# Performance work log

Hardware: AMD Instinct MI355X
Metric: run time of the kernel (lower is better)

Reference implementation:

```python
import jax, jax.numpy as jnp
import numpy as np

H = 4          # heads (hardcoded in original forward via shp=(4, ...))
B, G, D = 2, 2048, 128
KD = VD = 32   # key_dim = val_dim = embed_dim // n_heads
E = 128        # embed_dim


def setup_inputs() -> dict:
    key = jax.random.key(0)
    ks = jax.random.split(key, 10)
    s = lambda d: 1.0 / np.sqrt(d)
    return {
        "h": jax.random.normal(ks[0], (B, G, D), jnp.float32),
        "out_source_attn": jax.random.normal(ks[1], (H, B, G, G), jnp.float32),
        "Wq": jax.random.uniform(ks[2], (H, D, KD), jnp.float32, -s(KD), s(KD)),
        "Wk": jax.random.uniform(ks[3], (H, D, KD), jnp.float32, -s(KD), s(KD)),
        "Wv": jax.random.uniform(ks[4], (H, D, VD), jnp.float32, -s(VD), s(VD)),
        "Wout": jax.random.uniform(ks[5], (H, KD, E), jnp.float32, -s(E), s(E)),
        "w1": jax.random.uniform(ks[6], (8, 8), jnp.float32, -s(8), s(8)),
        "b1": jax.random.uniform(ks[7], (8,), jnp.float32, -s(8), s(8)),
        "w2": jax.random.uniform(ks[8], (4, 8), jnp.float32, -s(8), s(8)),
        "b2": jax.random.uniform(ks[9], (4,), jnp.float32, -s(4), s(4)),
    }


def reference(h, out_source_attn, Wq, Wk, Wv, Wout, w1, b1, w2, b2):
    # Per-head projections: (H, B, G, kd/vd)
    Q = jnp.einsum('bgd,hdk->hbgk', h, Wq)
    K = jnp.einsum('bgd,hdk->hbgk', h, Wk)
    V = jnp.einsum('bgd,hdv->hbgv', h, Wv)
    # QK^T scores concat with external attention source: (2H=8, B, G, G)
    scores = jnp.einsum('hbqk,hbpk->hbqp', Q, K)
    compat = jnp.concatenate([scores, out_source_attn], axis=0)
    # Per-score small MLP (Linear(8,8)->ReLU->Linear(8,4)) over channel dim
    x = compat.transpose(1, 2, 3, 0)                 # (B, G, G, 8)
    x = jax.nn.relu(x @ w1.T + b1) @ w2.T + b2       # (B, G, G, 4)
    attn = jax.nn.softmax(x.transpose(3, 0, 1, 2), axis=-1)  # (H, B, G, G)
    heads = jnp.einsum('hbqp,hbpv->hbqv', attn, V)   # (H, B, G, VD)
    out = jnp.einsum('hbqv,hve->bqe', heads, Wout)   # (B, G, E)
    return (out, out_source_attn)
```

## Files before the change

### kernel.cpp

```cpp
#include <hip/hip_runtime.h>

typedef __attribute__((ext_vector_type(8))) short bf16x8;
typedef __attribute__((ext_vector_type(4))) short bf16x4;
typedef __attribute__((ext_vector_type(4))) float f32x4;

#define OUT0 524288
#define SRC_CH_STRIDE 8388608
#define PART_HEAD 544
#define PART_SLICE 2176
#define NSLICE 8

__device__ __forceinline__ unsigned short f2bf(float x){
    unsigned u = __builtin_bit_cast(unsigned, x);
    u += 0x7FFFu + ((u >> 16) & 1u);
    return (unsigned short)(u >> 16);
}

__device__ __forceinline__ f32x4 mfma16x16x16_bf16(bf16x4 a, bf16x4 b, f32x4 c){
#if __has_builtin(__builtin_amdgcn_mfma_f32_16x16x16bf16_1k)
    return __builtin_amdgcn_mfma_f32_16x16x16bf16_1k(a, b, c, 0, 0, 0);
#else
    f32x4 d;
    asm volatile("v_mfma_f32_16x16x16_bf16 %0, %1, %2, %3"
                 : "=v"(d) : "v"(a), "v"(b), "v"(c));
    return d;
#endif
}

__global__ __launch_bounds__(256) void qkv_kernel(
    const float* __restrict__ hsrc,
    const float* __restrict__ Wq, const float* __restrict__ Wk, const float* __restrict__ Wv,
    unsigned short* __restrict__ Qb, unsigned short* __restrict__ Kb, unsigned short* __restrict__ Vt)
{
    __shared__ float hs[32*128];
    __shared__ float ws[128*32];
    const int t = threadIdx.x;
    const int g0 = blockIdx.x * 32;
    const int mat = blockIdx.y;
    const int mt = mat >> 2, head = mat & 3;
    {
        const float4* s = (const float4*)(hsrc + g0*128);
        float4* d = (float4*)hs;
        #pragma unroll
        for (int i=0;i<4;i++) d[t + i*256] = s[t + i*256];
        const float* W = (mt==0?Wq:(mt==1?Wk:Wv)) + head*4096;
        const float4* s2 = (const float4*)W;
        float4* d2 = (float4*)ws;
        #pragma unroll
        for (int i=0;i<4;i++) d2[t + i*256] = s2[t + i*256];
    }
    __syncthreads();
    const int r = t >> 3;
    const int k0 = (t & 7) * 4;
    float a0=0.f,a1=0.f,a2=0.f,a3=0.f;
    const float* hr = hs + r*128;
    #pragma unroll 8
    for (int d=0; d<128; d++){
        float hv = hr[d];
        float4 w4 = *(const float4*)(ws + d*32 + k0);
        a0 = fmaf(hv, w4.x, a0); a1 = fmaf(hv, w4.y, a1);
        a2 = fmaf(hv, w4.z, a2); a3 = fmaf(hv, w4.w, a3);
    }
    const int row_g = g0 + r;
    if (mt == 2){
        const int b = row_g >> 11, g = row_g & 2047;
        unsigned short* dst = Vt + ((b*128 + head*32 + k0) * 2048) + g;
        dst[0] = f2bf(a0); dst[2048] = f2bf(a1); dst[4096] = f2bf(a2); dst[6144] = f2bf(a3);
    } else {
        unsigned short* dst = (mt==0?Qb:Kb) + row_g*128 + head*32 + k0;
        dst[0]=f2bf(a0); dst[1]=f2bf(a1); dst[2]=f2bf(a2); dst[3]=f2bf(a3);
    }
}

__global__ __launch_bounds__(256, 2) void attn_kernel(
    const float* __restrict__ src,
    const unsigned short* __restrict__ Qb,
    const unsigned short* __restrict__ Kb,
    const unsigned short* __restrict__ Vt,
    const float* __restrict__ w1g, const float* __restrict__ b1g,
    const float* __restrict__ w2g, const float* __restrict__ b2g,
    float* __restrict__ part,
    float* __restrict__ out)
{
    __shared__ __align__(16) float wt[112];

    const int t = threadIdx.x;
    const int lane = t & 63;
    const int wv = t >> 6;
    const int quad = lane >> 4;
    const int lrow = lane & 15;
    const int qt = blockIdx.x * 4 + wv;
    const int q0 = qt * 16;
    const int b = blockIdx.y;
    const int s = blockIdx.z;
    const int pbase = s * (2048 / NSLICE);

    if (t < 64) wt[t] = w1g[t];
    else if (t < 72) wt[t] = b1g[t-64];
    else if (t < 104){ const int j = (t-72) >> 2, cc = (t-72) & 3; wt[t] = w2g[cc*8 + j]; }
    else if (t < 108) wt[t] = b2g[t-104];

    bf16x8 qf[4];
    {
        const unsigned short* Qrow = Qb + (b*2048 + q0 + lrow)*128 + quad*8;
        #pragma unroll
        for (int h=0; h<4; h++) qf[h] = *(const bf16x8*)(Qrow + h*32);
    }

    const int rowbase = (b*2048 + q0 + lrow)*2048;
    const long vbase  = (long)(b*128)*2048;

    f32x4 o[4][2];
    float mreg[4], lreg[4];
    #pragma unroll
    for (int h=0; h<4; h++){
        o[h][0] = (f32x4){0.f,0.f,0.f,0.f};
        o[h][1] = (f32x4){0.f,0.f,0.f,0.f};
        mreg[h] = -1e30f; lreg[h] = 0.f;
    }
    const f32x4 zero4 = {0.f,0.f,0.f,0.f};

    __syncthreads();

    for (int it = 0; it < (2048/NSLICE)/16; ++it){
        const int p0 = pbase + it*16;

        float xr[4][4];
        {
            float4 r4[4];
            #pragma unroll
            for (int ch=0; ch<4; ch++)
                r4[ch] = *(const float4*)(src + ch*SRC_CH_STRIDE + rowbase + p0 + quad*4);
            #pragma unroll
            for (int ch=0; ch<4; ch++)
                *(float4*)(out + OUT0 + ch*SRC_CH_STRIDE + rowbase + p0 + quad*4) = r4[ch];
            #pragma unroll
            for (int ch=0; ch<4; ch++){
                xr[ch][0]=r4[ch].x; xr[ch][1]=r4[ch].y; xr[ch][2]=r4[ch].z; xr[ch][3]=r4[ch].w;
            }
        }

        bf16x4 vf[4][2];
        #pragma unroll
        for (int h=0; h<4; h++){
            #pragma unroll
            for (int half=0; half<2; half++)
                vf[h][half] = *(const bf16x4*)(Vt + vbase + (long)(h*32 + half*16 + lrow)*2048 + p0 + quad*4);
        }

        f32x4 sc[4];
        {
            const unsigned short* Krow = Kb + (b*2048 + p0 + lrow)*128 + quad*8;
            #pragma unroll
            for (int h=0; h<4; h++){
                const bf16x8 kf = *(const bf16x8*)(Krow + h*32);
                sc[h] = __builtin_amdgcn_mfma_f32_16x16x32_bf16(kf, qf[h], zero4, 0, 0, 0);
            }
        }

        float z[4][4];
        #pragma unroll
        for (int cc=0; cc<4; cc++){
            const float bb = wt[104+cc];
            #pragma unroll
            for (int r=0; r<4; r++) z[cc][r] = bb;
        }
        #pragma unroll
        for (int j=0; j<8; j++){
            const float4 wa  = *(const float4*)(wt + j*8);
            const float4 wb  = *(const float4*)(wt + j*8 + 4);
            const float  bj  = wt[64+j];
            const float4 w2r = *(const float4*)(wt + 72 + j*4);
            #pragma unroll
            for (int r=0; r<4; r++){
                float v = bj;
                v = fmaf(wa.x, sc[0][r], v);
                v = fmaf(wa.y, sc[1][r], v);
                v = fmaf(wa.z, sc[2][r], v);
                v = fmaf(wa.w, sc[3][r], v);
                v = fmaf(wb.x, xr[0][r], v);
                v = fmaf(wb.y, xr[1][r], v);
                v = fmaf(wb.z, xr[2][r], v);
                v = fmaf(wb.w, xr[3][r], v);
                v = fmaxf(v, 0.f);
                z[0][r] = fmaf(w2r.x, v, z[0][r]);
                z[1][r] = fmaf(w2r.y, v, z[1][r]);
                z[2][r] = fmaf(w2r.z, v, z[2][r]);
                z[3][r] = fmaf(w2r.w, v, z[3][r]);
            }
        }

        #pragma unroll
        for (int h=0; h<4; h++){
            float mloc = fmaxf(fmaxf(z[h][0], z[h][1]), fmaxf(z[h][2], z[h][3]));
            mloc = fmaxf(mloc, __shfl_xor(mloc, 16));
            mloc = fmaxf(mloc, __shfl_xor(mloc, 32));
            const float mn = fmaxf(mreg[h], mloc);
            const float e0 = __expf(z[h][0] - mn);
            const float e1 = __expf(z[h][1] - mn);
            const float e2 = __expf(z[h][2] - mn);
            const float e3 = __expf(z[h][3] - mn);
            float ss = (e0 + e1) + (e2 + e3);
            ss += __shfl_xor(ss, 16);
            ss += __shfl_xor(ss, 32);
            const float alpha = __expf(mreg[h] - mn);
            mreg[h] = mn;
            lreg[h] = fmaf(lreg[h], alpha, ss);
            o[h][0] *= alpha;
            o[h][1] *= alpha;
            bf16x4 pf;
            pf[0] = (short)f2bf(e0); pf[1] = (short)f2bf(e1);
            pf[2] = (short)f2bf(e2); pf[3] = (short)f2bf(e3);
            o[h][0] = mfma16x16x16_bf16(vf[h][0], pf, o[h][0]);
            o[h][1] = mfma16x16x16_bf16(vf[h][1], pf, o[h][1]);
        }
    }

    #pragma unroll
    for (int h=0; h<4; h++){
        float* P = part + (((b*128 + qt)*NSLICE + s)*4 + h) * PART_HEAD;
        if (quad == 0){
            P[lrow]      = mreg[h];
            P[16 + lrow] = lreg[h];
        }
        *(f32x4*)(P + 32 + lrow*32 +      quad*4) = o[h][0];
        *(f32x4*)(P + 32 + lrow*32 + 16 + quad*4) = o[h][1];
    }
}

__global__ __launch_bounds__(256) void combine_kernel(
    const float* __restrict__ part,
    const float* __restrict__ Wout,
    float* __restrict__ out)
{
    __shared__ __align__(16) float O_lds[64*33];
    const int t = threadIdx.x;
    const int qt = blockIdx.x, b = blockIdx.y;

    if (t < 64){
        const int c = t >> 4, q = t & 15;
        const float* P0 = part + (((b*128 + qt)*NSLICE + 0)*4 + c) * PART_HEAD;
        float m[NSLICE];
        #pragma unroll
        for (int j=0;j<NSLICE;j++) m[j] = P0[j*PART_SLICE + q];
        float M = m[0];
        #pragma unroll
        for (int j=1;j<NSLICE;j++) M = fmaxf(M, m[j]);
        float w[NSLICE];
        float L = 0.f;
        #pragma unroll
        for (int j=0;j<NSLICE;j++){
            w[j] = __expf(m[j] - M);
            L = fmaf(P0[j*PART_SLICE + 16 + q], w[j], L);
        }
        float invL = 1.f / L;
        const float* O0 = P0 + 32 + q*32;
        float* dst = O_lds + t*33;
        #pragma unroll
        for (int v4 = 0; v4 < 8; v4++){
            float ax=0.f, ay=0.f, az=0.f, aw=0.f;
            #pragma unroll
            for (int j=0;j<NSLICE;j++){
                float4 a = *(const float4*)(O0 + j*PART_SLICE + v4*4);
                ax = fmaf(a.x, w[j], ax);
                ay = fmaf(a.y, w[j], ay);
                az = fmaf(a.z, w[j], az);
                aw = fmaf(a.w, w[j], aw);
            }
            dst[v4*4+0] = ax * invL;
            dst[v4*4+1] = ay * invL;
            dst[v4*4+2] = az * invL;
            dst[v4*4+3] = aw * invL;
        }
    }
    __syncthreads();

    {
        const int mq = t >> 4;
        const int e0 = (t & 15) * 8;
        float acc[8];
        #pragma unroll
        for (int i=0;i<8;i++) acc[i]=0.f;
        #pragma unroll
        for (int cc=0; cc<4; cc++){
            const float* OhRow = O_lds + (cc*16 + mq)*33;
            const float* Wrow = Wout + cc*32*128 + e0;
            #pragma unroll 4
            for (int v=0; v<32; v++){
                float ov = OhRow[v];
                float4 wA = *(const float4*)(Wrow + v*128);
                float4 wB = *(const float4*)(Wrow + v*128 + 4);
                acc[0]=fmaf(ov,wA.x,acc[0]); acc[1]=fmaf(ov,wA.y,acc[1]);
                acc[2]=fmaf(ov,wA.z,acc[2]); acc[3]=fmaf(ov,wA.w,acc[3]);
                acc[4]=fmaf(ov,wB.x,acc[4]); acc[5]=fmaf(ov,wB.y,acc[5]);
                acc[6]=fmaf(ov,wB.z,acc[6]); acc[7]=fmaf(ov,wB.w,acc[7]);
            }
        }
        float* op = out + (b*2048 + qt*16 + mq)*128 + e0;
        float4 oA; oA.x=acc[0]; oA.y=acc[1]; oA.z=acc[2]; oA.w=acc[3];
        float4 oB; oB.x=acc[4]; oB.y=acc[5]; oB.z=acc[6]; oB.w=acc[7];
        *(float4*)op = oA;
        *(float4*)(op+4) = oB;
    }
}

extern "C" void kernel_launch(void* const* d_in, const int* in_sizes, int n_in,
                              void* d_out, int out_size, void* d_ws, size_t ws_size,
                              hipStream_t stream) {
    const float* h    = (const float*)d_in[0];
    const float* src  = (const float*)d_in[1];
    const float* Wq   = (const float*)d_in[2];
    const float* Wk   = (const float*)d_in[3];
    const float* Wv   = (const float*)d_in[4];
    const float* Wout = (const float*)d_in[5];
    const float* w1   = (const float*)d_in[6];
    const float* b1   = (const float*)d_in[7];
    const float* w2   = (const float*)d_in[8];
    const float* b2   = (const float*)d_in[9];
    float* out = (float*)d_out;

    unsigned short* Qb = (unsigned short*)d_ws;
    unsigned short* Kb = Qb + 524288;
    unsigned short* Vt = Kb + 524288;
    float* part = (float*)((char*)d_ws + 3*1048576);

    qkv_kernel<<<dim3(128,12), 256, 0, stream>>>(h, Wq, Wk, Wv, Qb, Kb, Vt);
    attn_kernel<<<dim3(32,2,NSLICE), 256, 0, stream>>>(src, Qb, Kb, Vt, w1, b1, w2, b2, part, out);
    combine_kernel<<<dim3(128,2), 256, 0, stream>>>(part, Wout, out);
}
```

Measured before the change: 387.9 us.

## Double-buffer source attention loads across 32-column pairs of subtiles

Restructures the main loop to prefetch the next 32 columns of out_source_attn into registers, using two ping-pong buffers, while the current pair of 16-column subtiles is computed. The copy-out store and the loads are issued ahead of the MLP and softmax work to hide global memory latency. This adds register pressure from holding 32 extra floats per buffer, which could reduce occupancy.

```diff
diff --git a/kernel.cpp b/kernel.cpp
--- a/kernel.cpp
+++ b/kernel.cpp
@@ -120,34 +120,21 @@
     }
     const f32x4 zero4 = {0.f,0.f,0.f,0.f};
 
-    __syncthreads();
-
-    for (int it = 0; it < (2048/NSLICE)/16; ++it){
-        const int p0 = pbase + it*16;
-
-        float xr[4][4];
-        {
-            float4 r4[4];
+    auto pairload = [&](float4 (&buf)[2][4], int pb){
+        #pragma unroll
+        for (int s2=0; s2<2; s2++)
             #pragma unroll
             for (int ch=0; ch<4; ch++)
-                r4[ch] = *(const float4*)(src + ch*SRC_CH_STRIDE + rowbase + p0 + quad*4);
+                buf[s2][ch] = *(const float4*)(src + ch*SRC_CH_STRIDE + rowbase + pb + s2*16 + quad*4);
+    };
+    auto pairstore = [&](float4 (&buf)[2][4], int pb){
+        #pragma unroll
+        for (int s2=0; s2<2; s2++)
             #pragma unroll
             for (int ch=0; ch<4; ch++)
-                *(float4*)(out + OUT0 + ch*SRC_CH_STRIDE + rowbase + p0 + quad*4) = r4[ch];
-            #pragma unroll
-            for (int ch=0; ch<4; ch++){
-                xr[ch][0]=r4[ch].x; xr[ch][1]=r4[ch].y; xr[ch][2]=r4[ch].z; xr[ch][3]=r4[ch].w;
-            }
-        }
-
-        bf16x4 vf[4][2];
-        #pragma unroll
-        for (int h=0; h<4; h++){
-            #pragma unroll
-            for (int half=0; half<2; half++)
-                vf[h][half] = *(const bf16x4*)(Vt + vbase + (long)(h*32 + half*16 + lrow)*2048 + p0 + quad*4);
-        }
-
+                *(float4*)(out + OUT0 + ch*SRC_CH_STRIDE + rowbase + pb + s2*16 + quad*4) = buf[s2][ch];
+    };
+    auto subtile = [&](int p0, const float4* x4){
         f32x4 sc[4];
         {
             const unsigned short* Krow = Kb + (b*2048 + p0 + lrow)*128 + quad*8;
@@ -157,7 +144,18 @@
                 sc[h] = __builtin_amdgcn_mfma_f32_16x16x32_bf16(kf, qf[h], zero4, 0, 0, 0);
             }
         }
-
+        bf16x4 vf[4][2];
+        #pragma unroll
+        for (int h=0; h<4; h++)
+            #pragma unroll
+            for (int hf=0; hf<2; hf++)
+                vf[h][hf] = *(const bf16x4*)(Vt + vbase + (long)(h*32 + hf*16 + lrow)*2048 + p0 + quad*4);
+
+        float xr[4][4];
+        #pragma unroll
+        for (int ch=0; ch<4; ch++){
+            xr[ch][0]=x4[ch].x; xr[ch][1]=x4[ch].y; xr[ch][2]=x4[ch].z; xr[ch][3]=x4[ch].w;
+        }
         float z[4][4];
         #pragma unroll
         for (int cc=0; cc<4; cc++){
@@ -189,7 +187,6 @@
                 z[3][r] = fmaf(w2r.w, v, z[3][r]);
             }
         }
-
         #pragma unroll
         for (int h=0; h<4; h++){
             float mloc = fmaxf(fmaxf(z[h][0], z[h][1]), fmaxf(z[h][2], z[h][3]));
@@ -214,6 +211,24 @@
             o[h][0] = mfma16x16x16_bf16(vf[h][0], pf, o[h][0]);
             o[h][1] = mfma16x16x16_bf16(vf[h][1], pf, o[h][1]);
         }
+    };
+
+    float4 bufA[2][4], bufB[2][4];
+    pairload(bufA, pbase);
+
+    __syncthreads();
+
+    for (int ip = 0; ip < 8; ip += 2){
+        const int pb0 = pbase + ip*32;
+        const int pb1 = pb0 + 32;
+        pairload(bufB, pb1);
+        pairstore(bufA, pb0);
+        subtile(pb0,      bufA[0]);
+        subtile(pb0 + 16, bufA[1]);
+        if (ip < 6) pairload(bufA, pb1 + 32);
+        pairstore(bufB, pb1);
+        subtile(pb1,      bufB[0]);
+        subtile(pb1 + 16, bufB[1]);
     }
 
     #pragma unroll
```

Result: slower. 649.6 us (+67.5%).
